# Kernel tuning notes

Hardware: AMD Instinct MI355X
Metric: run time of the kernel (lower is better)

Reference implementation:

```python
import jax, jax.numpy as jnp
import numpy as np

B, T, D, H = 2, 2048, 1024, 16
HD = D // H


def setup_inputs() -> dict:
    key = jax.random.key(0)
    ks = jax.random.split(key, 9)
    s = 1.0 / np.sqrt(D)
    return {
        "x": jax.random.normal(ks[0], (B, T, D), dtype=jnp.float32),
        "Wq": jax.random.normal(ks[1], (D, D), dtype=jnp.float32) * s,
        "bq": jnp.zeros((D,), dtype=jnp.float32),
        "Wk": jax.random.normal(ks[2], (D, D), dtype=jnp.float32) * s,
        "bk": jnp.zeros((D,), dtype=jnp.float32),
        "Wv": jax.random.normal(ks[3], (D, D), dtype=jnp.float32) * s,
        "bv": jnp.zeros((D,), dtype=jnp.float32),
        "Wo": jax.random.normal(ks[4], (D, D), dtype=jnp.float32) * s,
        "bo": jnp.zeros((D,), dtype=jnp.float32),
    }


def reference(x, Wq, bq, Wk, bk, Wv, bv, Wo, bo):
    b, t, d = x.shape
    # projections, split heads: (b, h, t, hd)
    def heads(y):
        return y.reshape(b, t, H, HD).transpose(0, 2, 1, 3)
    Q = heads(x @ Wq + bq)
    K = heads(x @ Wk + bk)
    V = heads(x @ Wv + bv)
    # scores scaled by sqrt(d) (full embed dim, faithful to source)
    score = jnp.einsum("bhid,bhjd->bhij", Q, K) / jnp.sqrt(jnp.float32(d))
    causal = jnp.triu(jnp.ones((t, t), dtype=bool), k=1)  # (t, t)
    score = jnp.where(causal, jnp.float32(-1e10), score)
    # FAITHFUL quirk: softmax over the HEAD axis (torch dim=1 of [b,h,t,t])
    weight = jax.nn.softmax(score, axis=1)
    out = jnp.einsum("bhij,bhjd->bhid", weight, V)
    out = out.transpose(0, 2, 1, 3).reshape(b, t, d)
    return out @ Wo + bo
```

## Files before the change

kernel.cpp:

```cpp
#include <hip/hip_runtime.h>
#include <hip/hip_bf16.h>

#define B_ 2
#define T_ 2048
#define D_ 1024
#define H_ 16

typedef __attribute__((ext_vector_type(8))) short bf16x8;
typedef __attribute__((ext_vector_type(4))) short bf16x4;
typedef __attribute__((ext_vector_type(4))) float f32x4;

__device__ __forceinline__ unsigned pack_bf16(float x, float y) {
  unsigned xb = __float_as_uint(x), yb = __float_as_uint(y);
  xb += 0x7fffu + ((xb >> 16) & 1u);
  yb += 0x7fffu + ((yb >> 16) & 1u);
  return (xb >> 16) | (yb & 0xffff0000u);
}
__device__ __forceinline__ unsigned short f2b(float x) {
  unsigned u = __float_as_uint(x);
  u += 0x7fffu + ((u >> 16) & 1u);
  return (unsigned short)(u >> 16);
}
__device__ __forceinline__ float blo(unsigned u) { return __uint_as_float(u << 16); }
__device__ __forceinline__ float bhi(unsigned u) { return __uint_as_float(u & 0xffff0000u); }

__device__ __forceinline__ void gld_lds16(const unsigned short* g, unsigned short* l) {
  __builtin_amdgcn_global_load_lds(
      (const __attribute__((address_space(1))) unsigned int*)g,
      (__attribute__((address_space(3))) unsigned int*)l, 16, 0, 0);
}

__global__ __launch_bounds__(256) void wtrans(const float* __restrict__ W0, const float* __restrict__ W1,
                                              const float* __restrict__ W2, const float* __restrict__ W3,
                                              unsigned short* __restrict__ T0, unsigned short* __restrict__ T1,
                                              unsigned short* __restrict__ T2, unsigned short* __restrict__ T3) {
  const int z = blockIdx.z;
  const float* W = z == 0 ? W0 : z == 1 ? W1 : z == 2 ? W2 : W3;
  unsigned short* T = z == 0 ? T0 : z == 1 ? T1 : z == 2 ? T2 : T3;
  __shared__ unsigned short t[64][72];
  const int k0 = blockIdx.x << 6, n0 = blockIdx.y << 6;
  const int r = threadIdx.x >> 2, c16 = (threadIdx.x & 3) << 4;
#pragma unroll
  for (int e = 0; e < 4; ++e) {
    const float4 v = *(const float4*)&W[(size_t)(k0 + r) * 1024 + n0 + c16 + e * 4];
    t[r][c16 + e * 4 + 0] = f2b(v.x);
    t[r][c16 + e * 4 + 1] = f2b(v.y);
    t[r][c16 + e * 4 + 2] = f2b(v.z);
    t[r][c16 + e * 4 + 3] = f2b(v.w);
  }
  __syncthreads();
  unsigned short o[16];
#pragma unroll
  for (int e = 0; e < 16; ++e) o[e] = t[c16 + e][r];
  unsigned short* dst = &T[(size_t)(n0 + r) * 1024 + k0 + c16];
  *(uint4*)&dst[0] = *(uint4*)&o[0];
  *(uint4*)&dst[8] = *(uint4*)&o[8];
}

__global__ __launch_bounds__(256) void xconv(const float* __restrict__ x, unsigned short* __restrict__ xb) {
  const int i = (blockIdx.x * 256 + threadIdx.x) * 8;
  const float4 a = *(const float4*)&x[i];
  const float4 b = *(const float4*)&x[i + 4];
  uint4 o;
  o.x = pack_bf16(a.x, a.y);
  o.y = pack_bf16(a.z, a.w);
  o.z = pack_bf16(b.x, b.y);
  o.w = pack_bf16(b.z, b.w);
  *(uint4*)&xb[i] = o;
}

template <bool BF16OUT>
__global__ __launch_bounds__(256) void gemm_mfma(const unsigned short* __restrict__ A,
                                                 const unsigned short* __restrict__ B0,
                                                 const unsigned short* __restrict__ B1,
                                                 const unsigned short* __restrict__ B2,
                                                 const float* __restrict__ bi0, const float* __restrict__ bi1,
                                                 const float* __restrict__ bi2,
                                                 void* __restrict__ Y0, void* __restrict__ Y1,
                                                 void* __restrict__ Y2) {
  const int z = blockIdx.z;
  const unsigned short* Bt = z == 0 ? B0 : z == 1 ? B1 : B2;
  const float* bias = z == 0 ? bi0 : z == 1 ? bi1 : bi2;
  void* Y = z == 0 ? Y0 : z == 1 ? Y1 : Y2;
  __shared__ unsigned short As[8192];
  __shared__ unsigned short Bs[8192];
  const int tid = threadIdx.x;
  const int m0 = blockIdx.y << 7, n0 = blockIdx.x << 7;
  const int w = tid >> 6, l = tid & 63, g = l >> 4, c = l & 15;
  const int wm = (w >> 1) << 6, wn = (w & 1) << 6;
  const int srow = tid >> 3;
  const int skel = ((tid & 7) ^ (srow & 7)) << 3;
  const unsigned short* ga = &A[(size_t)(m0 + srow) * 1024 + skel];
  const unsigned short* gb = &Bt[(size_t)(n0 + srow) * 1024 + skel];
  unsigned short* la = &As[tid << 3];
  unsigned short* lb = &Bs[tid << 3];
  f32x4 acc[4][4];
#pragma unroll
  for (int i = 0; i < 4; ++i)
#pragma unroll
    for (int j = 0; j < 4; ++j) acc[i][j] = {0.f, 0.f, 0.f, 0.f};
  for (int k0 = 0; k0 < 1024; k0 += 64) {
    __syncthreads();
#pragma unroll
    for (int a = 0; a < 4; ++a) {
      gld_lds16(ga + (size_t)(a << 5) * 1024 + k0, la + (a << 11));
      gld_lds16(gb + (size_t)(a << 5) * 1024 + k0, lb + (a << 11));
    }
    __syncthreads();
#pragma unroll
    for (int kc = 0; kc < 2; ++kc) {
      bf16x8 af[4], bfr[4];
#pragma unroll
      for (int mf = 0; mf < 4; ++mf) {
        const int m = wm + (mf << 4) + c;
        af[mf] = *(const bf16x8*)&As[((m << 6) + (kc << 5) + (g << 3)) ^ ((m & 7) << 3)];
      }
#pragma unroll
      for (int nf = 0; nf < 4; ++nf) {
        const int n = wn + (nf << 4) + c;
        bfr[nf] = *(const bf16x8*)&Bs[((n << 6) + (kc << 5) + (g << 3)) ^ ((n & 7) << 3)];
      }
#pragma unroll
      for (int mf = 0; mf < 4; ++mf)
#pragma unroll
        for (int nf = 0; nf < 4; ++nf)
          acc[mf][nf] = __builtin_amdgcn_mfma_f32_16x16x32_bf16(af[mf], bfr[nf], acc[mf][nf], 0, 0, 0);
    }
  }
#pragma unroll
  for (int nf = 0; nf < 4; ++nf) {
    const int n = n0 + wn + (nf << 4) + c;
    const float bb = bias[n];
#pragma unroll
    for (int mf = 0; mf < 4; ++mf) {
      const int mrow = m0 + wm + (mf << 4) + (g << 2);
#pragma unroll
      for (int r = 0; r < 4; ++r) {
        const float val = acc[mf][nf][r] + bb;
        if (BF16OUT)
          ((unsigned short*)Y)[((size_t)(mrow + r) << 10) + n] = f2b(val);
        else
          ((float*)Y)[((size_t)(mrow + r) << 10) + n] = val;
      }
    }
  }
}

__global__ __launch_bounds__(256) void gemm_vt(const unsigned short* __restrict__ A,
                                               const unsigned short* __restrict__ Bt,
                                               const float* __restrict__ bias,
                                               unsigned short* __restrict__ Vt) {
  __shared__ unsigned short As[8192];
  __shared__ unsigned short Bs[8192];
  __shared__ unsigned short sm[128][136];
  const int tid = threadIdx.x;
  const int m0 = blockIdx.y << 7, n0 = blockIdx.x << 7;
  const int w = tid >> 6, l = tid & 63, g = l >> 4, c = l & 15;
  const int wm = (w >> 1) << 6, wn = (w & 1) << 6;
  const int srow = tid >> 3;
  const int skel = ((tid & 7) ^ (srow & 7)) << 3;
  const unsigned short* ga = &A[(size_t)(m0 + srow) * 1024 + skel];
  const unsigned short* gb = &Bt[(size_t)(n0 + srow) * 1024 + skel];
  unsigned short* la = &As[tid << 3];
  unsigned short* lb = &Bs[tid << 3];
  f32x4 acc[4][4];
#pragma unroll
  for (int i = 0; i < 4; ++i)
#pragma unroll
    for (int j = 0; j < 4; ++j) acc[i][j] = {0.f, 0.f, 0.f, 0.f};
  for (int k0 = 0; k0 < 1024; k0 += 64) {
    __syncthreads();
#pragma unroll
    for (int a = 0; a < 4; ++a) {
      gld_lds16(ga + (size_t)(a << 5) * 1024 + k0, la + (a << 11));
      gld_lds16(gb + (size_t)(a << 5) * 1024 + k0, lb + (a << 11));
    }
    __syncthreads();
#pragma unroll
    for (int kc = 0; kc < 2; ++kc) {
      bf16x8 af[4], bfr[4];
#pragma unroll
      for (int mf = 0; mf < 4; ++mf) {
        const int m = wm + (mf << 4) + c;
        af[mf] = *(const bf16x8*)&As[((m << 6) + (kc << 5) + (g << 3)) ^ ((m & 7) << 3)];
      }
#pragma unroll
      for (int nf = 0; nf < 4; ++nf) {
        const int n = wn + (nf << 4) + c;
        bfr[nf] = *(const bf16x8*)&Bs[((n << 6) + (kc << 5) + (g << 3)) ^ ((n & 7) << 3)];
      }
#pragma unroll
      for (int mf = 0; mf < 4; ++mf)
#pragma unroll
        for (int nf = 0; nf < 4; ++nf)
          acc[mf][nf] = __builtin_amdgcn_mfma_f32_16x16x32_bf16(af[mf], bfr[nf], acc[mf][nf], 0, 0, 0);
    }
  }
  __syncthreads();
#pragma unroll
  for (int nf = 0; nf < 4; ++nf) {
    const int nl = wn + (nf << 4) + c;
    const float bb = bias[n0 + nl];
#pragma unroll
    for (int mf = 0; mf < 4; ++mf) {
      const int ml = wm + (mf << 4) + (g << 2);
      uint2 o;
      o.x = pack_bf16(acc[mf][nf][0] + bb, acc[mf][nf][1] + bb);
      o.y = pack_bf16(acc[mf][nf][2] + bb, acc[mf][nf][3] + bb);
      *(uint2*)&sm[nl][ml] = o;
    }
  }
  __syncthreads();
  const int bb2 = m0 >> 11, mr0 = m0 & 2047;
#pragma unroll
  for (int it = 0; it < 8; ++it) {
    const int u = tid + (it << 8);
    const int ns = u >> 4, mc = (u & 15) << 3;
    *(uint4*)&Vt[(((size_t)((bb2 << 10) + n0 + ns)) << 11) + mr0 + mc] = *(const uint4*)&sm[ns][mc];
  }
}

__global__ __launch_bounds__(256) void vblk32t(const unsigned short* __restrict__ Vt,
                                               float* __restrict__ Blk) {
  const int b = blockIdx.x >> 6, t = blockIdx.x & 63;
#pragma unroll
  for (int dd = 0; dd < 4; ++dd) {
    const int d = threadIdx.x + (dd << 8);
    const unsigned short* vr = &Vt[(((size_t)((b << 10) + d)) << 11) + (t << 5)];
    float s = 0.f;
#pragma unroll
    for (int qq = 0; qq < 4; ++qq) {
      const uint2 v0 = *(const uint2*)&vr[qq << 3];
      const uint2 v1 = *(const uint2*)&vr[(qq << 3) + 4];
      s += blo(v0.x) + bhi(v0.x) + blo(v0.y) + bhi(v0.y);
      s += blo(v1.x) + bhi(v1.x) + blo(v1.y) + bhi(v1.y);
    }
    Blk[(((size_t)((b << 6) + t)) << 10) + d] = s;
  }
}

__global__ __launch_bounds__(256) void vsuffix32(const float* __restrict__ Blk, float* __restrict__ Suf) {
  const int idx = blockIdx.x * 256 + threadIdx.x;
  const int b = idx >> 10, d = idx & 1023;
  float s = 0.f;
  Suf[((size_t)(b * 65 + 64) << 10) + d] = 0.f;
  for (int t = 63; t >= 0; --t) {
    s += Blk[((size_t)((b << 6) + t) << 10) + d];
    Suf[((size_t)(b * 65 + t) << 10) + d] = s;
  }
}

__global__ __launch_bounds__(1024, 4) void attn_v19(const unsigned short* __restrict__ Qb,
                                                    const unsigned short* __restrict__ Kb,
                                                    const unsigned short* __restrict__ Vt,
                                                    unsigned short* __restrict__ P0,
                                                    unsigned short* __restrict__ P1,
                                                    unsigned short* __restrict__ P2,
                                                    unsigned short* __restrict__ P3) {
  __shared__ unsigned short Ks[2][16 * 1024];
  __shared__ unsigned short Vs[2][1024 * 16];
  __shared__ f32x4 Sx[2][8][64];

  const int combo = blockIdx.x;
  const int b = combo & 1, s = combo >> 1;
  const int qy = 63 - blockIdx.y;
  const int tid = threadIdx.x;
  const int w = tid >> 6, l = tid & 63, g = l >> 4, c = l & 15;
  const int isub = w >> 3, hp = w & 7;
  const float SC = 0.04508422f;
  unsigned short* AOp = s == 0 ? P0 : s == 1 ? P1 : s == 2 ? P2 : P3;

  const int krow0 = tid >> 7, kc8 = tid & 127;
  const int kscc0 = kc8 ^ (krow0 & 7);
  const int krow1 = krow0 + 8;
  const int kscc1 = kc8 ^ (krow1 & 7);
  const unsigned short* kp0 = &Kb[(((size_t)((b << 11) + krow0)) << 10) + (kscc0 << 3)];
  const unsigned short* kp1 = &Kb[(((size_t)((b << 11) + krow1)) << 10) + (kscc1 << 3)];
  const int vd0 = tid >> 1, vjc = tid & 1;
  const int vjo0 = ((vjc << 1) ^ (((vd0 >> 2) & 1) << 1)) << 2;
  const int vd1 = vd0 + 512;
  const int vjo1 = ((vjc << 1) ^ (((vd1 >> 2) & 1) << 1)) << 2;
  const unsigned short* vp0 = &Vt[(((size_t)((b << 10) + vd0)) << 11) + vjo0];
  const unsigned short* vp1 = &Vt[(((size_t)((b << 10) + vd1)) << 11) + vjo1];

#pragma unroll
  for (int ph = 0; ph < 2; ++ph) {
    const int q = ph ? (63 - qy) : qy;
    const int nt16 = (q + 1) << 1;
    const int i0w = (q << 5) + (isub << 4);
    const int ib = i0w + c;

    const unsigned short* qbase =
        &Qb[((size_t)((b << 11) + i0w + c) << 10) + (hp << 7) + (g << 3)];
    bf16x8 qf[4];
    qf[0] = *(const bf16x8*)&qbase[0];
    qf[1] = *(const bf16x8*)&qbase[32];
    qf[2] = *(const bf16x8*)&qbase[64];
    qf[3] = *(const bf16x8*)&qbase[96];

    f32x4 acc[2][4];
#pragma unroll
    for (int hh = 0; hh < 2; ++hh)
#pragma unroll
      for (int cc = 0; cc < 4; ++cc) acc[hh][cc] = {0.f, 0.f, 0.f, 0.f};

#pragma unroll
    for (int e = 0; e < 2; ++e) {
      const int eh = e ? (7 - s) : s;
      const int lo = eh << 4;
      const int hi = (lo + 16) < nt16 ? (lo + 16) : nt16;
      if (lo >= hi) continue;

      {
        const size_t ko = ((size_t)lo << 14);
        gld_lds16(kp0 + ko, &Ks[0][tid << 3]);
        gld_lds16(kp1 + ko, &Ks[0][(tid + 1024) << 3]);
        const int jo = lo << 4;
        gld_lds16(vp0 + jo, &Vs[0][tid << 3]);
        gld_lds16(vp1 + jo, &Vs[0][(tid + 1024) << 3]);
      }
      __syncthreads();

      for (int ts = lo; ts < hi; ++ts) {
        const int cur = (ts - lo) & 1;
        if (ts + 1 < hi) {
          const size_t ko = ((size_t)(ts + 1) << 14);
          gld_lds16(kp0 + ko, &Ks[cur ^ 1][tid << 3]);
          gld_lds16(kp1 + ko, &Ks[cur ^ 1][(tid + 1024) << 3]);
          const int jo = (ts + 1) << 4;
          gld_lds16(vp0 + jo, &Vs[cur ^ 1][tid << 3]);
          gld_lds16(vp1 + jo, &Vs[cur ^ 1][(tid + 1024) << 3]);
        }
        const int j0 = ts << 4;
        const int kx = c & 7;
        f32x4 ex[2];
        f32x4 ps = {0.f, 0.f, 0.f, 0.f};
#pragma unroll
        for (int hh = 0; hh < 2; ++hh) {
          const int hc = ((hp << 1) + hh) << 3;
          const bf16x8 k0 = *(const bf16x8*)&Ks[cur][((c << 7) + ((hc + g) ^ kx)) << 3];
          const bf16x8 k1 = *(const bf16x8*)&Ks[cur][((c << 7) + ((hc + 4 + g) ^ kx)) << 3];
          f32x4 a = {0.f, 0.f, 0.f, 0.f};
          a = __builtin_amdgcn_mfma_f32_16x16x32_bf16(k0, qf[2 * hh], a, 0, 0, 0);
          a = __builtin_amdgcn_mfma_f32_16x16x32_bf16(k1, qf[2 * hh + 1], a, 0, 0, 0);
#pragma unroll
          for (int r = 0; r < 4; ++r) ex[hh][r] = exp2f(a[r] * SC);
          ps += ex[hh];
        }
        Sx[isub][hp][l] = ps;
        asm volatile("s_waitcnt lgkmcnt(0)" ::: "memory");
        __builtin_amdgcn_s_barrier();
        __builtin_amdgcn_sched_barrier(0);
        f32x4 sum = Sx[isub][0][l];
#pragma unroll
        for (int d8 = 1; d8 < 8; ++d8) sum += Sx[isub][d8][l];
        f32x4 inv;
#pragma unroll
        for (int r = 0; r < 4; ++r) inv[r] = __builtin_amdgcn_rcpf(sum[r]);
        float wv[2][4];
        if (j0 + 15 <= i0w) {
#pragma unroll
          for (int hh = 0; hh < 2; ++hh)
#pragma unroll
            for (int r = 0; r < 4; ++r) wv[hh][r] = ex[hh][r] * inv[r];
        } else {
          const int jb = j0 + (g << 2);
#pragma unroll
          for (int hh = 0; hh < 2; ++hh)
#pragma unroll
            for (int r = 0; r < 4; ++r)
              wv[hh][r] = (jb + r > ib) ? 0.0625f : ex[hh][r] * inv[r];
        }
#pragma unroll
        for (int hh = 0; hh < 2; ++hh) {
          union { bf16x4 v; unsigned u[2]; } pa;
          pa.u[0] = pack_bf16(wv[hh][0], wv[hh][1]);
          pa.u[1] = pack_bf16(wv[hh][2], wv[hh][3]);
#pragma unroll
          for (int cc = 0; cc < 4; ++cc) {
            const int d = (((hp << 1) + hh) << 6) + (cc << 4) + c;
            const int up = g ^ (((d >> 2) & 1) << 1);
            union { bf16x4 v; unsigned u[2]; } vf;
            *(uint2*)&vf = *(const uint2*)&Vs[cur][(d << 4) + (up << 2)];
            acc[hh][cc] =
                __builtin_amdgcn_mfma_f32_16x16x16bf16_1k(pa.v, vf.v, acc[hh][cc], 0, 0, 0);
          }
        }
        __syncthreads();
      }
    }
#pragma unroll
    for (int hh = 0; hh < 2; ++hh)
#pragma unroll
      for (int cc = 0; cc < 4; ++cc) {
        const int d = (((hp << 1) + hh) << 6) + (cc << 4) + c;
#pragma unroll
        for (int r = 0; r < 4; ++r)
          AOp[((size_t)((b << 11) + i0w + (g << 2) + r) << 10) + d] = f2b(acc[hh][cc][r]);
      }
  }
}

__global__ __launch_bounds__(256) void aocvt(const unsigned short* __restrict__ P0,
                                             const unsigned short* __restrict__ P1,
                                             const unsigned short* __restrict__ P2,
                                             const unsigned short* __restrict__ P3,
                                             const float* __restrict__ Suf,
                                             unsigned short* __restrict__ AOb) {
  const int i = (blockIdx.x * 256 + threadIdx.x) << 3;
  const int m = i >> 10;
  const int b = m >> 11;
  const int sufidx = ((m & 2047) >> 5) + 1;
  const int d0 = i & 1023;
  const float* sp = &Suf[((size_t)(b * 65 + sufidx) << 10) + d0];
  const uint4 v0 = *(const uint4*)&P0[i];
  const uint4 v1 = *(const uint4*)&P1[i];
  const uint4 v2 = *(const uint4*)&P2[i];
  const uint4 v3 = *(const uint4*)&P3[i];
  const float4 s0 = *(const float4*)&sp[0];
  const float4 s1 = *(const float4*)&sp[4];
  uint4 o;
  o.x = pack_bf16(blo(v0.x) + blo(v1.x) + blo(v2.x) + blo(v3.x) + 0.0625f * s0.x,
                  bhi(v0.x) + bhi(v1.x) + bhi(v2.x) + bhi(v3.x) + 0.0625f * s0.y);
  o.y = pack_bf16(blo(v0.y) + blo(v1.y) + blo(v2.y) + blo(v3.y) + 0.0625f * s0.z,
                  bhi(v0.y) + bhi(v1.y) + bhi(v2.y) + bhi(v3.y) + 0.0625f * s0.w);
  o.z = pack_bf16(blo(v0.z) + blo(v1.z) + blo(v2.z) + blo(v3.z) + 0.0625f * s1.x,
                  bhi(v0.z) + bhi(v1.z) + bhi(v2.z) + bhi(v3.z) + 0.0625f * s1.y);
  o.w = pack_bf16(blo(v0.w) + blo(v1.w) + blo(v2.w) + blo(v3.w) + 0.0625f * s1.z,
                  bhi(v0.w) + bhi(v1.w) + bhi(v2.w) + bhi(v3.w) + 0.0625f * s1.w);
  *(uint4*)&AOb[i] = o;
}

extern "C" void kernel_launch(void* const* d_in, const int* in_sizes, int n_in,
                              void* d_out, int out_size, void* d_ws, size_t ws_size,
                              hipStream_t stream) {
  (void)in_sizes; (void)n_in; (void)out_size; (void)ws_size;
  const float* x = (const float*)d_in[0];
  const float* Wq = (const float*)d_in[1];
  const float* bq = (const float*)d_in[2];
  const float* Wk = (const float*)d_in[3];
  const float* bk = (const float*)d_in[4];
  const float* Wv = (const float*)d_in[5];
  const float* bv = (const float*)d_in[6];
  const float* Wo = (const float*)d_in[7];
  const float* bo = (const float*)d_in[8];
  float* out = (float*)d_out;
  char* ws = (char*)d_ws;

  const size_t MB = 1024 * 1024;
  unsigned short* xb  = (unsigned short*)(ws);
  unsigned short* Qb  = (unsigned short*)(ws + 8 * MB);
  unsigned short* Kb  = (unsigned short*)(ws + 16 * MB);
  unsigned short* AOP1 = (unsigned short*)(ws + 24 * MB);
  unsigned short* Vt  = (unsigned short*)(ws + 32 * MB);
  unsigned short* Wqt = (unsigned short*)(ws + 40 * MB);
  unsigned short* Wkt = (unsigned short*)(ws + 42 * MB);
  unsigned short* Wvt = (unsigned short*)(ws + 44 * MB);
  unsigned short* Wot = (unsigned short*)(ws + 46 * MB);
  unsigned short* AOP2 = (unsigned short*)(ws + 48 * MB);
  unsigned short* AOP3 = (unsigned short*)(ws + 56 * MB);
  float* Blk = (float*)(ws + 40 * MB);
  float* Suf = (float*)(ws + 40 * MB + 512 * 1024);
  unsigned short* AOP0 = xb;
  unsigned short* AOb = Qb;

  hipLaunchKernelGGL(wtrans, dim3(16, 16, 4), dim3(256), 0, stream,
                     Wq, Wk, Wv, Wo, Wqt, Wkt, Wvt, Wot);
  hipLaunchKernelGGL(xconv, dim3(2048), dim3(256), 0, stream, x, xb);
  hipLaunchKernelGGL((gemm_mfma<true>), dim3(8, 32, 2), dim3(256), 0, stream,
                     xb, Wqt, Wkt, Wkt, bq, bk, bk, (void*)Qb, (void*)Kb, (void*)Kb);
  hipLaunchKernelGGL(gemm_vt, dim3(8, 32), dim3(256), 0, stream, xb, Wvt, bv, Vt);
  hipLaunchKernelGGL(vblk32t, dim3(128), dim3(256), 0, stream, Vt, Blk);
  hipLaunchKernelGGL(vsuffix32, dim3(8), dim3(256), 0, stream, Blk, Suf);
  hipLaunchKernelGGL(attn_v19, dim3(8, 32), dim3(1024), 0, stream,
                     Qb, Kb, Vt, AOP0, AOP1, AOP2, AOP3);
  hipLaunchKernelGGL(aocvt, dim3(2048), dim3(256), 0, stream,
                     AOP0, AOP1, AOP2, AOP3, Suf, AOb);
  hipLaunchKernelGGL((gemm_mfma<false>), dim3(8, 32, 1), dim3(256), 0, stream,
                     AOb, Wot, Wot, Wot, bo, bo, bo, (void*)out, (void*)out, (void*)out);
}
```

Measured before the change: 193.6 us.

## Use LDS atomics for head-sum reduction, fuse V suffix kernels, use hardware bf16 pack

Three changes. The cross-wave softmax denominator is now accumulated with LDS float atomics into a double-buffered slot, replacing eight-way stores plus reads, and one wave zeroes the next buffer. The V block-sum and suffix-scan kernels merge into one 8-block kernel, which drops a launch but has each thread read a full V row serially. The software bf16 rounding in the attention loop is replaced by the v_cvt_pk_bf16_f32 instruction. LDS atomic contention and the low-parallelism suffix kernel could offset these gains.

```diff
diff --git a/kernel.cpp b/kernel.cpp
--- a/kernel.cpp
+++ b/kernel.cpp
@@ -15,6 +15,11 @@
   xb += 0x7fffu + ((xb >> 16) & 1u);
   yb += 0x7fffu + ((yb >> 16) & 1u);
   return (xb >> 16) | (yb & 0xffff0000u);
+}
+__device__ __forceinline__ unsigned cvt_pk(float lo, float hi) {
+  unsigned r;
+  asm("v_cvt_pk_bf16_f32 %0, %1, %2" : "=v"(r) : "v"(lo), "v"(hi));
+  return r;
 }
 __device__ __forceinline__ unsigned short f2b(float x) {
   unsigned u = __float_as_uint(x);
@@ -220,37 +225,28 @@
   }
 }
 
-__global__ __launch_bounds__(256) void vblk32t(const unsigned short* __restrict__ Vt,
-                                               float* __restrict__ Blk) {
-  const int b = blockIdx.x >> 6, t = blockIdx.x & 63;
-#pragma unroll
-  for (int dd = 0; dd < 4; ++dd) {
-    const int d = threadIdx.x + (dd << 8);
-    const unsigned short* vr = &Vt[(((size_t)((b << 10) + d)) << 11) + (t << 5)];
-    float s = 0.f;
-#pragma unroll
-    for (int qq = 0; qq < 4; ++qq) {
-      const uint2 v0 = *(const uint2*)&vr[qq << 3];
-      const uint2 v1 = *(const uint2*)&vr[(qq << 3) + 4];
-      s += blo(v0.x) + bhi(v0.x) + blo(v0.y) + bhi(v0.y);
-      s += blo(v1.x) + bhi(v1.x) + blo(v1.y) + bhi(v1.y);
-    }
-    Blk[(((size_t)((b << 6) + t)) << 10) + d] = s;
-  }
-}
-
-__global__ __launch_bounds__(256) void vsuffix32(const float* __restrict__ Blk, float* __restrict__ Suf) {
-  const int idx = blockIdx.x * 256 + threadIdx.x;
-  const int b = idx >> 10, d = idx & 1023;
+__global__ __launch_bounds__(256) void vsuf(const unsigned short* __restrict__ Vt,
+                                            float* __restrict__ Suf) {
+  const int b = blockIdx.x >> 2;
+  const int d = ((blockIdx.x & 3) << 8) + threadIdx.x;
+  const unsigned short* vr = &Vt[((size_t)((b << 10) + d)) << 11];
   float s = 0.f;
   Suf[((size_t)(b * 65 + 64) << 10) + d] = 0.f;
   for (int t = 63; t >= 0; --t) {
-    s += Blk[((size_t)((b << 6) + t) << 10) + d];
+    float ts = 0.f;
+#pragma unroll
+    for (int qq = 0; qq < 4; ++qq) {
+      const uint2 v0 = *(const uint2*)&vr[(t << 5) + (qq << 3)];
+      const uint2 v1 = *(const uint2*)&vr[(t << 5) + (qq << 3) + 4];
+      ts += blo(v0.x) + bhi(v0.x) + blo(v0.y) + bhi(v0.y);
+      ts += blo(v1.x) + bhi(v1.x) + blo(v1.y) + bhi(v1.y);
+    }
+    s += ts;
     Suf[((size_t)(b * 65 + t) << 10) + d] = s;
   }
 }
 
-__global__ __launch_bounds__(1024, 4) void attn_v19(const unsigned short* __restrict__ Qb,
+__global__ __launch_bounds__(1024, 4) void attn_v20(const unsigned short* __restrict__ Qb,
                                                     const unsigned short* __restrict__ Kb,
                                                     const unsigned short* __restrict__ Vt,
                                                     unsigned short* __restrict__ P0,
@@ -259,7 +255,7 @@
                                                     unsigned short* __restrict__ P3) {
   __shared__ unsigned short Ks[2][16 * 1024];
   __shared__ unsigned short Vs[2][1024 * 16];
-  __shared__ f32x4 Sx[2][8][64];
+  __shared__ float SxA[2][2][64][4];
 
   const int combo = blockIdx.x;
   const int b = combo & 1, s = combo >> 1;
@@ -311,6 +307,10 @@
       const int hi = (lo + 16) < nt16 ? (lo + 16) : nt16;
       if (lo >= hi) continue;
 
+      if (hp == 0) {
+        *(f32x4*)&SxA[0][isub][l][0] = (f32x4){0.f, 0.f, 0.f, 0.f};
+        *(f32x4*)&SxA[1][isub][l][0] = (f32x4){0.f, 0.f, 0.f, 0.f};
+      }
       {
         const size_t ko = ((size_t)lo << 14);
         gld_lds16(kp0 + ko, &Ks[0][tid << 3]);
@@ -321,6 +321,7 @@
       }
       __syncthreads();
 
+      int sxb = 0;
       for (int ts = lo; ts < hi; ++ts) {
         const int cur = (ts - lo) & 1;
         if (ts + 1 < hi) {
@@ -347,16 +348,17 @@
           for (int r = 0; r < 4; ++r) ex[hh][r] = exp2f(a[r] * SC);
           ps += ex[hh];
         }
-        Sx[isub][hp][l] = ps;
+#pragma unroll
+        for (int r = 0; r < 4; ++r) unsafeAtomicAdd(&SxA[sxb][isub][l][r], ps[r]);
         asm volatile("s_waitcnt lgkmcnt(0)" ::: "memory");
         __builtin_amdgcn_s_barrier();
         __builtin_amdgcn_sched_barrier(0);
-        f32x4 sum = Sx[isub][0][l];
-#pragma unroll
-        for (int d8 = 1; d8 < 8; ++d8) sum += Sx[isub][d8][l];
+        const f32x4 sum = *(const f32x4*)&SxA[sxb][isub][l][0];
         f32x4 inv;
 #pragma unroll
         for (int r = 0; r < 4; ++r) inv[r] = __builtin_amdgcn_rcpf(sum[r]);
+        if (hp == 0) *(f32x4*)&SxA[sxb ^ 1][isub][l][0] = (f32x4){0.f, 0.f, 0.f, 0.f};
+        sxb ^= 1;
         float wv[2][4];
         if (j0 + 15 <= i0w) {
 #pragma unroll
@@ -374,8 +376,8 @@
 #pragma unroll
         for (int hh = 0; hh < 2; ++hh) {
           union { bf16x4 v; unsigned u[2]; } pa;
-          pa.u[0] = pack_bf16(wv[hh][0], wv[hh][1]);
-          pa.u[1] = pack_bf16(wv[hh][2], wv[hh][3]);
+          pa.u[0] = cvt_pk(wv[hh][0], wv[hh][1]);
+          pa.u[1] = cvt_pk(wv[hh][2], wv[hh][3]);
 #pragma unroll
           for (int cc = 0; cc < 4; ++cc) {
             const int d = (((hp << 1) + hh) << 6) + (cc << 4) + c;
@@ -459,8 +461,7 @@
   unsigned short* Wot = (unsigned short*)(ws + 46 * MB);
   unsigned short* AOP2 = (unsigned short*)(ws + 48 * MB);
   unsigned short* AOP3 = (unsigned short*)(ws + 56 * MB);
-  float* Blk = (float*)(ws + 40 * MB);
-  float* Suf = (float*)(ws + 40 * MB + 512 * 1024);
+  float* Suf = (float*)(ws + 40 * MB);
   unsigned short* AOP0 = xb;
   unsigned short* AOb = Qb;
 
@@ -470,9 +471,8 @@
   hipLaunchKernelGGL((gemm_mfma<true>), dim3(8, 32, 2), dim3(256), 0, stream,
                      xb, Wqt, Wkt, Wkt, bq, bk, bk, (void*)Qb, (void*)Kb, (void*)Kb);
   hipLaunchKernelGGL(gemm_vt, dim3(8, 32), dim3(256), 0, stream, xb, Wvt, bv, Vt);
-  hipLaunchKernelGGL(vblk32t, dim3(128), dim3(256), 0, stream, Vt, Blk);
-  hipLaunchKernelGGL(vsuffix32, dim3(8), dim3(256), 0, stream, Blk, Suf);
-  hipLaunchKernelGGL(attn_v19, dim3(8, 32), dim3(1024), 0, stream,
+  hipLaunchKernelGGL(vsuf, dim3(8), dim3(256), 0, stream, Vt, Suf);
+  hipLaunchKernelGGL(attn_v20, dim3(8, 32), dim3(1024), 0, stream,
                      Qb, Kb, Vt, AOP0, AOP1, AOP2, AOP3);
   hipLaunchKernelGGL(aocvt, dim3(2048), dim3(256), 0, stream,
                      AOP0, AOP1, AOP2, AOP3, Suf, AOb);
```

Result: slower. 365.4 us (+88.7%).
